# Performance work log

Measured on AMD Instinct MI355X. Metric: run time of the kernel, lower is better.

## Reference

```python
import jax, jax.numpy as jnp
import numpy as np

NUM_GROUPS = 32
EPS = 1e-5


def setup_inputs() -> dict:
    key = jax.random.key(0)
    ks = jax.random.split(key, 11)
    B, C, H, W = 4, 512, 64, 64
    s = 1.0 / np.sqrt(C)
    inp = {
        "x": jax.random.normal(ks[0], (B, C, H, W), dtype=jnp.float32),
        "gn_w": jnp.ones((C,), jnp.float32),
        "gn_b": jnp.zeros((C,), jnp.float32),
        "wq": jax.random.uniform(ks[1], (C, C), jnp.float32, -s, s),
        "bq": jax.random.uniform(ks[2], (C,), jnp.float32, -s, s),
        "wk": jax.random.uniform(ks[3], (C, C), jnp.float32, -s, s),
        "bk": jax.random.uniform(ks[4], (C,), jnp.float32, -s, s),
        "wv": jax.random.uniform(ks[5], (C, C), jnp.float32, -s, s),
        "bv": jax.random.uniform(ks[6], (C,), jnp.float32, -s, s),
        "wo": jax.random.uniform(ks[7], (C, C), jnp.float32, -s, s),
        "bo": jax.random.uniform(ks[8], (C,), jnp.float32, -s, s),
    }
    return inp


def reference(x, gn_w, gn_b, wq, bq, wk, bk, wv, bv, wo, bo):
    B, C, H, W = x.shape
    HW = H * W
    # GroupNorm(32, C)
    g = x.reshape(B, NUM_GROUPS, C // NUM_GROUPS, H, W)
    mu = jnp.mean(g, axis=(2, 3, 4), keepdims=True)
    var = jnp.var(g, axis=(2, 3, 4), keepdims=True)
    h = ((g - mu) * jax.lax.rsqrt(var + EPS)).reshape(B, C, H, W)
    h = h * gn_w[None, :, None, None] + gn_b[None, :, None, None]
    # Faithful to original: .view (reshape), NOT permute -> (B, HW, C)
    h = h.reshape(B, HW, C)
    q = h @ wq.T + bq  # (B, HW, C)
    k = h @ wk.T + bk
    v = h @ wv.T + bv
    # Faithful: reshape (not transpose) to (B, C, HW)
    q = q.reshape(B, C, HW)
    k = k.reshape(B, C, HW)
    v = v.reshape(B, C, HW)
    # attn: (B, HW, HW)
    attn = jnp.einsum('bcn,bcm->bnm', q, k)
    attn = jax.nn.softmax(attn, axis=-1)
    # out: (B, C, HW) = v @ attn^T
    out = jnp.einsum('bcm,bnm->bcn', v, attn)
    # transpose to (B, HW, C), out-proj, then reshape back
    out = jnp.swapaxes(out, 1, 2) @ wo.T + bo
    out = out.reshape(B, C, H, W)
    return out + x
```

## Files before the change

### kernel.cpp

```cpp
#include <hip/hip_runtime.h>
#include <hip/hip_fp16.h>
#include <math.h>

constexpr int BATCH = 4;
constexpr int HWDIM = 4096;
constexpr long CNT   = 2097152;
constexpr long ACNT  = 16777216;
constexpr int GSIZE = 65536;
constexpr float GN_EPS = 1e-5f;

typedef __attribute__((ext_vector_type(8))) _Float16 f16x8;
typedef __attribute__((ext_vector_type(4))) float f32x4;

__device__ __forceinline__ unsigned pkf16(float a, float b) {
  __half ha = __float2half(a), hb = __float2half(b);
  return (unsigned)__half_as_ushort(ha) | ((unsigned)__half_as_ushort(hb) << 16);
}
__device__ __forceinline__ float2 up2(unsigned u) {
  __half2 h = *(__half2*)&u;
  return __half22float2(h);
}
__device__ __forceinline__ void gl_lds16(const void* g, void* l) {
  __builtin_amdgcn_global_load_lds((const __attribute__((address_space(1))) unsigned*)g,
                                   (__attribute__((address_space(3))) unsigned*)l, 16, 0, 0);
}

__global__ void gn_stats_kernel(const float* __restrict__ x,
                                float* __restrict__ mu, float* __restrict__ rs) {
  const int grp = blockIdx.x;
  const float4* p = (const float4*)(x + (long)grp * GSIZE);
  float s = 0.f, q = 0.f;
  for (int i = threadIdx.x; i < GSIZE / 4; i += 256) {
    float4 v = p[i];
    s += (v.x + v.y) + (v.z + v.w);
    q += (v.x * v.x + v.y * v.y) + (v.z * v.z + v.w * v.w);
  }
  #pragma unroll
  for (int o = 32; o > 0; o >>= 1) { s += __shfl_xor(s, o, 64); q += __shfl_xor(q, o, 64); }
  __shared__ float ls[4], lq[4];
  if ((threadIdx.x & 63) == 0) { ls[threadIdx.x >> 6] = s; lq[threadIdx.x >> 6] = q; }
  __syncthreads();
  if (threadIdx.x == 0) {
    float S = (ls[0] + ls[1]) + (ls[2] + ls[3]);
    float Q = (lq[0] + lq[1]) + (lq[2] + lq[3]);
    float m = S * (1.f / GSIZE);
    float var = Q * (1.f / GSIZE) - m * m;
    mu[grp] = m; rs[grp] = rsqrtf(var + GN_EPS);
  }
}

__global__ void gn_norm_f16(const float* __restrict__ x,
                            const float* __restrict__ mu, const float* __restrict__ rs,
                            const float* __restrict__ gw, const float* __restrict__ gb,
                            unsigned short* __restrict__ h) {
  long i = ((long)blockIdx.x * 256 + threadIdx.x) * 4;
  int c   = (int)((i >> 12) & 511);
  int grp = (int)(i >> 16);
  float m = mu[grp], r = rs[grp];
  float w = gw[c] * r;
  float bia = gb[c] - m * w;
  float4 v = *(const float4*)(x + i);
  *(uint2*)(h + i) = (uint2){ pkf16(v.x * w + bia, v.y * w + bia),
                              pkf16(v.z * w + bia, v.w * w + bia) };
}

__global__ void wcvt(const float* __restrict__ w0, const float* __restrict__ w1,
                     const float* __restrict__ w2, const float* __restrict__ w3,
                     unsigned short* __restrict__ o) {
  const float* src = blockIdx.y == 0 ? w0 : blockIdx.y == 1 ? w1 : blockIdx.y == 2 ? w2 : w3;
  long e = ((long)blockIdx.x * 256 + threadIdx.x) * 4;
  float4 v = *(const float4*)(src + e);
  *(uint2*)(o + (long)blockIdx.y * 262144 + e) = (uint2){ pkf16(v.x, v.y), pkf16(v.z, v.w) };
}

__launch_bounds__(256)
__global__ void proj_qkv(const unsigned short* __restrict__ A, const unsigned short* __restrict__ WF,
                         const float* __restrict__ bq, const float* __restrict__ bk,
                         const float* __restrict__ bv, unsigned short* __restrict__ outq) {
  __shared__ __align__(16) unsigned short LB[32768];
  const int z = blockIdx.z;
  const unsigned short* W = WF + (long)z * 262144;
  const float* bias = z == 0 ? bq : z == 1 ? bk : bv;
  unsigned short* outp = outq + (long)z * 8388608;
  const int m0 = blockIdx.x * 128, n0 = blockIdx.y * 128;
  const int t = threadIdx.x, lane = t & 63, w = t >> 6, wm = w & 1, wn = w >> 1;

  f32x4 acc[4][4];
  #pragma unroll
  for (int i = 0; i < 4; i++)
    #pragma unroll
    for (int j = 0; j < 4; j++) acc[i][j] = (f32x4){0.f, 0.f, 0.f, 0.f};

  auto stage = [&](int buf, int k0) {
    unsigned short* As = LB + buf * 16384;
    unsigned short* Bs = As + 8192;
    #pragma unroll
    for (int fbi = 0; fbi < 4; fbi++) {
      int fb = w * 4 + fbi;
      int row = (fb >> 1) * 16 + (lane & 15);
      int g   = (fb & 1) * 4 + (lane >> 4);
      gl_lds16(A + (long)(m0 + row) * 512 + k0 + g * 8, &As[(fb * 64) << 3]);
      gl_lds16(W + (long)(n0 + row) * 512 + k0 + g * 8, &Bs[(fb * 64) << 3]);
    }
  };

  stage(0, 0);
  __syncthreads();
  for (int k0 = 0; k0 < 512; k0 += 64) {
    const int cur = (k0 >> 6) & 1;
    if (k0 + 64 < 512) stage(cur ^ 1, k0 + 64);
    const unsigned short* As = LB + cur * 16384;
    const unsigned short* Bs = As + 8192;
    #pragma unroll
    for (int kk = 0; kk < 2; kk++) {
      f16x8 a[4], b[4];
      #pragma unroll
      for (int i = 0; i < 4; i++)
        a[i] = *(const f16x8*)&As[(((wm * 4 + i) * 2 + kk) * 64 + lane) << 3];
      #pragma unroll
      for (int j = 0; j < 4; j++)
        b[j] = *(const f16x8*)&Bs[(((wn * 4 + j) * 2 + kk) * 64 + lane) << 3];
      #pragma unroll
      for (int i = 0; i < 4; i++)
        #pragma unroll
        for (int j = 0; j < 4; j++)
          acc[i][j] = __builtin_amdgcn_mfma_f32_16x16x32_f16(a[i], b[j], acc[i][j], 0, 0, 0);
    }
    __syncthreads();
  }

  const int lm = lane & 15, quad = lane >> 4;
  #pragma unroll
  for (int i = 0; i < 4; i++)
    #pragma unroll
    for (int j = 0; j < 4; j++) {
      int rr = wm * 64 + i * 16 + quad * 4;
      int cc = wn * 64 + j * 16 + lm;
      float bb = bias[n0 + cc];
      #pragma unroll
      for (int r = 0; r < 4; r++)
        LB[(rr + r) * 136 + cc] = __half_as_ushort(__float2half(acc[i][j][r] + bb));
    }
  __syncthreads();
  #pragma unroll
  for (int k = 0; k < 8; k++) {
    int ro = k * 16 + (t >> 4), col = (t & 15) * 8;
    uint4 vv = *(const uint4*)&LB[ro * 136 + col];
    *(uint4*)(outp + (long)(m0 + ro) * 512 + n0 + col) = vv;
  }
}

__launch_bounds__(256)
__global__ void proj_out(const unsigned short* __restrict__ A, const unsigned short* __restrict__ W,
                         const float* __restrict__ bias, const float* __restrict__ res,
                         float* __restrict__ outv) {
  __shared__ __align__(16) unsigned short LB[32768];
  const int m0 = blockIdx.x * 128, n0 = blockIdx.y * 128;
  const int t = threadIdx.x, lane = t & 63, w = t >> 6, wm = w & 1, wn = w >> 1;

  f32x4 acc[4][4];
  #pragma unroll
  for (int i = 0; i < 4; i++)
    #pragma unroll
    for (int j = 0; j < 4; j++) acc[i][j] = (f32x4){0.f, 0.f, 0.f, 0.f};

  auto stage = [&](int buf, int k0) {
    unsigned short* As = LB + buf * 16384;
    unsigned short* Bs = As + 8192;
    #pragma unroll
    for (int fbi = 0; fbi < 4; fbi++) {
      int fb = w * 4 + fbi;
      int row = (fb >> 1) * 16 + (lane & 15);
      int g   = (fb & 1) * 4 + (lane >> 4);
      gl_lds16(A + (long)(m0 + row) * 512 + k0 + g * 8, &As[(fb * 64) << 3]);
      gl_lds16(W + (long)(n0 + row) * 512 + k0 + g * 8, &Bs[(fb * 64) << 3]);
    }
  };

  stage(0, 0);
  __syncthreads();
  for (int k0 = 0; k0 < 512; k0 += 64) {
    const int cur = (k0 >> 6) & 1;
    if (k0 + 64 < 512) stage(cur ^ 1, k0 + 64);
    const unsigned short* As = LB + cur * 16384;
    const unsigned short* Bs = As + 8192;
    #pragma unroll
    for (int kk = 0; kk < 2; kk++) {
      f16x8 a[4], b[4];
      #pragma unroll
      for (int i = 0; i < 4; i++)
        a[i] = *(const f16x8*)&As[(((wm * 4 + i) * 2 + kk) * 64 + lane) << 3];
      #pragma unroll
      for (int j = 0; j < 4; j++)
        b[j] = *(const f16x8*)&Bs[(((wn * 4 + j) * 2 + kk) * 64 + lane) << 3];
      #pragma unroll
      for (int i = 0; i < 4; i++)
        #pragma unroll
        for (int j = 0; j < 4; j++)
          acc[i][j] = __builtin_amdgcn_mfma_f32_16x16x32_f16(a[i], b[j], acc[i][j], 0, 0, 0);
    }
    __syncthreads();
  }

  const int lm = lane & 15, quad = lane >> 4;
  #pragma unroll
  for (int i = 0; i < 4; i++)
    #pragma unroll
    for (int j = 0; j < 4; j++) {
      int nn = m0 + wm * 64 + i * 16 + quad * 4;
      int cc = n0 + wn * 64 + j * 16 + lm;
      float bb = bias[cc];
      #pragma unroll
      for (int r = 0; r < 4; r++) {
        long idx = (long)(nn + r) * 512 + cc;
        outv[idx] = acc[i][j][r] + bb + res[idx];
      }
    }
}

__global__ void transpose_f16(const unsigned short* __restrict__ qb,
                              const unsigned short* __restrict__ kb,
                              unsigned short* __restrict__ tr) {
  __shared__ __align__(16) unsigned short ld[64 * 72];
  const int zb = blockIdx.z;
  const int b = zb >> 1;
  const unsigned short* in = (zb & 1 ? kb : qb) + (long)b * CNT;
  unsigned short* o = tr + (long)b * 2 * CNT + (zb & 1 ? CNT : 0);
  const int n0 = blockIdx.x * 64, c0 = blockIdx.y * 64;
  const int t = threadIdx.x;
  unsigned* ld32 = (unsigned*)ld;
  {
    const int p = t >> 3, cg = t & 7;
    uint4 r0 = *(const uint4*)(in + (long)(c0 + 2 * p) * 4096 + n0 + 8 * cg);
    uint4 r1 = *(const uint4*)(in + (long)(c0 + 2 * p + 1) * 4096 + n0 + 8 * cg);
    unsigned aw[4] = { r0.x, r0.y, r0.z, r0.w };
    unsigned bw[4] = { r1.x, r1.y, r1.z, r1.w };
    #pragma unroll
    for (int i = 0; i < 4; i++) {
      ld32[(8 * cg + 2 * i) * 36 + p]     = (aw[i] & 0xFFFFu) | (bw[i] << 16);
      ld32[(8 * cg + 2 * i + 1) * 36 + p] = (aw[i] >> 16) | (bw[i] & 0xFFFF0000u);
    }
  }
  __syncthreads();
  {
    const int n = t >> 2, cg2 = t & 3;
    uint4 o0 = *(const uint4*)(ld + n * 72 + 16 * cg2);
    uint4 o1 = *(const uint4*)(ld + n * 72 + 16 * cg2 + 8);
    *(uint4*)(o + (long)(n0 + n) * 512 + c0 + 16 * cg2)     = o0;
    *(uint4*)(o + (long)(n0 + n) * 512 + c0 + 16 * cg2 + 8) = o1;
  }
}

__launch_bounds__(256)
__global__ void qk_f16(const unsigned short* __restrict__ tr, unsigned short* __restrict__ attn) {
  __shared__ __align__(16) unsigned short LB[32768];
  const int b = blockIdx.z;
  const unsigned short* qT = tr + (long)b * 2 * CNT;
  const unsigned short* kT = qT + CNT;
  unsigned short* attnb = attn + (long)b * ACNT;
  const int n0 = blockIdx.x * 128, m0 = blockIdx.y * 128;
  const int t = threadIdx.x, lane = t & 63, w = t >> 6, wm = w & 1, wn = w >> 1;

  f32x4 acc[4][4];
  #pragma unroll
  for (int i = 0; i < 4; i++)
    #pragma unroll
    for (int j = 0; j < 4; j++) acc[i][j] = (f32x4){0.f, 0.f, 0.f, 0.f};

  auto stage = [&](int buf, int k0) {
    unsigned short* As = LB + buf * 16384;
    unsigned short* Bs = As + 8192;
    #pragma unroll
    for (int fbi = 0; fbi < 4; fbi++) {
      int fb = w * 4 + fbi;
      int row = (fb >> 1) * 16 + (lane & 15);
      int g   = (fb & 1) * 4 + (lane >> 4);
      gl_lds16(qT + (long)(n0 + row) * 512 + k0 + g * 8, &As[(fb * 64) << 3]);
      gl_lds16(kT + (long)(m0 + row) * 512 + k0 + g * 8, &Bs[(fb * 64) << 3]);
    }
  };

  stage(0, 0);
  __syncthreads();
  for (int k0 = 0; k0 < 512; k0 += 64) {
    const int cur = (k0 >> 6) & 1;
    if (k0 + 64 < 512) stage(cur ^ 1, k0 + 64);
    const unsigned short* As = LB + cur * 16384;
    const unsigned short* Bs = As + 8192;
    #pragma unroll
    for (int kk = 0; kk < 2; kk++) {
      f16x8 a[4], b[4];
      #pragma unroll
      for (int i = 0; i < 4; i++)
        a[i] = *(const f16x8*)&As[(((wm * 4 + i) * 2 + kk) * 64 + lane) << 3];
      #pragma unroll
      for (int j = 0; j < 4; j++)
        b[j] = *(const f16x8*)&Bs[(((wn * 4 + j) * 2 + kk) * 64 + lane) << 3];
      #pragma unroll
      for (int i = 0; i < 4; i++)
        #pragma unroll
        for (int j = 0; j < 4; j++)
          acc[i][j] = __builtin_amdgcn_mfma_f32_16x16x32_f16(a[i], b[j], acc[i][j], 0, 0, 0);
    }
    __syncthreads();
  }

  const int lm = lane & 15, quad = lane >> 4;
  #pragma unroll
  for (int i = 0; i < 4; i++)
    #pragma unroll
    for (int j = 0; j < 4; j++) {
      int rr = wm * 64 + i * 16 + quad * 4;
      int cc = wn * 64 + j * 16 + lm;
      #pragma unroll
      for (int r = 0; r < 4; r++)
        LB[(rr + r) * 136 + cc] = __half_as_ushort(__float2half(acc[i][j][r]));
    }
  __syncthreads();
  #pragma unroll
  for (int k = 0; k < 8; k++) {
    int ro = k * 16 + (t >> 4), col = (t & 15) * 8;
    uint4 vv = *(const uint4*)&LB[ro * 136 + col];
    *(uint4*)(attnb + (long)(n0 + ro) * 4096 + m0 + col) = vv;
  }
}

__global__ void softmax_f16ip(unsigned short* __restrict__ attn) {
  unsigned short* p = attn + (long)blockIdx.x * HWDIM;
  const int t = threadIdx.x;
  uint4 u0 = *(const uint4*)(p + t * 16);
  uint4 u1 = *(const uint4*)(p + t * 16 + 8);
  float v[16];
  {
    unsigned uu[8] = { u0.x, u0.y, u0.z, u0.w, u1.x, u1.y, u1.z, u1.w };
    #pragma unroll
    for (int i = 0; i < 8; i++) { float2 f = up2(uu[i]); v[2*i] = f.x; v[2*i+1] = f.y; }
  }
  float mx = -1e30f;
  #pragma unroll
  for (int i = 0; i < 16; i++) mx = fmaxf(mx, v[i]);
  #pragma unroll
  for (int o = 32; o > 0; o >>= 1) mx = fmaxf(mx, __shfl_xor(mx, o, 64));
  __shared__ float rmax[4], rsum[4];
  if ((t & 63) == 0) rmax[t >> 6] = mx;
  __syncthreads();
  mx = fmaxf(fmaxf(rmax[0], rmax[1]), fmaxf(rmax[2], rmax[3]));
  float s = 0.f;
  #pragma unroll
  for (int i = 0; i < 16; i++) { v[i] = __expf(v[i] - mx); s += v[i]; }
  #pragma unroll
  for (int o = 32; o > 0; o >>= 1) s += __shfl_xor(s, o, 64);
  if ((t & 63) == 0) rsum[t >> 6] = s;
  __syncthreads();
  s = (rsum[0] + rsum[1]) + (rsum[2] + rsum[3]);
  float inv = 1.f / s;
  uint4 w0, w1;
  w0.x = pkf16(v[0]*inv,  v[1]*inv);  w0.y = pkf16(v[2]*inv,  v[3]*inv);
  w0.z = pkf16(v[4]*inv,  v[5]*inv);  w0.w = pkf16(v[6]*inv,  v[7]*inv);
  w1.x = pkf16(v[8]*inv,  v[9]*inv);  w1.y = pkf16(v[10]*inv, v[11]*inv);
  w1.z = pkf16(v[12]*inv, v[13]*inv); w1.w = pkf16(v[14]*inv, v[15]*inv);
  *(uint4*)(p + t * 16)     = w0;
  *(uint4*)(p + t * 16 + 8) = w1;
}

__launch_bounds__(256)
__global__ void pv_f16(const unsigned short* __restrict__ P, const unsigned short* __restrict__ V,
                       unsigned short* __restrict__ ot) {
  __shared__ __align__(16) unsigned short LB[32768];
  const int b = blockIdx.z;
  const unsigned short* Pb = P + (long)b * ACNT;
  const unsigned short* Vb = V + (long)b * CNT;
  unsigned short* Ob = ot + (long)b * CNT;
  const int n0 = blockIdx.x * 128, c0 = blockIdx.y * 128;
  const int t = threadIdx.x, lane = t & 63, w = t >> 6, wm = w & 1, wn = w >> 1;

  f32x4 acc[4][4];
  #pragma unroll
  for (int i = 0; i < 4; i++)
    #pragma unroll
    for (int j = 0; j < 4; j++) acc[i][j] = (f32x4){0.f, 0.f, 0.f, 0.f};

  auto stage = [&](int buf, int k0) {
    unsigned short* As = LB + buf * 16384;
    unsigned short* Bs = As + 8192;
    #pragma unroll
    for (int fbi = 0; fbi < 4; fbi++) {
      int fb = w * 4 + fbi;
      int row = (fb >> 1) * 16 + (lane & 15);
      int g   = (fb & 1) * 4 + (lane >> 4);
      gl_lds16(Pb + (long)(n0 + row) * 4096 + k0 + g * 8, &As[(fb * 64) << 3]);
      gl_lds16(Vb + (long)(c0 + row) * 4096 + k0 + g * 8, &Bs[(fb * 64) << 3]);
    }
  };

  stage(0, 0);
  __syncthreads();
  for (int k0 = 0; k0 < 4096; k0 += 64) {
    const int cur = (k0 >> 6) & 1;
    if (k0 + 64 < 4096) stage(cur ^ 1, k0 + 64);
    const unsigned short* As = LB + cur * 16384;
    const unsigned short* Bs = As + 8192;
    #pragma unroll
    for (int kk = 0; kk < 2; kk++) {
      f16x8 a[4], b[4];
      #pragma unroll
      for (int i = 0; i < 4; i++)
        a[i] = *(const f16x8*)&As[(((wm * 4 + i) * 2 + kk) * 64 + lane) << 3];
      #pragma unroll
      for (int j = 0; j < 4; j++)
        b[j] = *(const f16x8*)&Bs[(((wn * 4 + j) * 2 + kk) * 64 + lane) << 3];
      #pragma unroll
      for (int i = 0; i < 4; i++)
        #pragma unroll
        for (int j = 0; j < 4; j++)
          acc[i][j] = __builtin_amdgcn_mfma_f32_16x16x32_f16(a[i], b[j], acc[i][j], 0, 0, 0);
    }
    __syncthreads();
  }

  const int lm = lane & 15, quad = lane >> 4;
  #pragma unroll
  for (int i = 0; i < 4; i++)
    #pragma unroll
    for (int j = 0; j < 4; j++) {
      int rr = wm * 64 + i * 16 + quad * 4;
      int cc = wn * 64 + j * 16 + lm;
      #pragma unroll
      for (int r = 0; r < 4; r++)
        LB[(rr + r) * 136 + cc] = __half_as_ushort(__float2half(acc[i][j][r]));
    }
  __syncthreads();
  #pragma unroll
  for (int k = 0; k < 8; k++) {
    int ro = k * 16 + (t >> 4), col = (t & 15) * 8;
    uint4 vv = *(const uint4*)&LB[ro * 136 + col];
    *(uint4*)(Ob + (long)(n0 + ro) * 512 + c0 + col) = vv;
  }
}

extern "C" void kernel_launch(void* const* d_in, const int* in_sizes, int n_in,
                              void* d_out, int out_size, void* d_ws, size_t ws_size,
                              hipStream_t stream) {
  (void)in_sizes; (void)n_in; (void)out_size; (void)ws_size;
  const float* x  = (const float*)d_in[0];
  const float* gw = (const float*)d_in[1];
  const float* gb = (const float*)d_in[2];
  const float* wq = (const float*)d_in[3];
  const float* bq = (const float*)d_in[4];
  const float* wk = (const float*)d_in[5];
  const float* bk = (const float*)d_in[6];
  const float* wv = (const float*)d_in[7];
  const float* bv = (const float*)d_in[8];
  const float* wo = (const float*)d_in[9];
  const float* bo = (const float*)d_in[10];
  float* out = (float*)d_out;

  unsigned short* attn = (unsigned short*)d_ws;
  unsigned short* h    = attn;
  unsigned short* qf   = attn + 4 * ACNT;
  unsigned short* kf   = qf + 8388608;
  unsigned short* vf   = kf + 8388608;
  unsigned short* tr   = vf + 8388608;
  unsigned short* ot   = tr + 16777216;
  unsigned short* wf   = ot + 8388608;
  float* mu = (float*)(wf + 1048576);
  float* rs = mu + 128;

  gn_stats_kernel<<<dim3(128), dim3(256), 0, stream>>>(x, mu, rs);
  gn_norm_f16<<<dim3(8192), dim3(256), 0, stream>>>(x, mu, rs, gw, gb, h);
  wcvt<<<dim3(256, 4), dim3(256), 0, stream>>>(wq, wk, wv, wo, wf);

  proj_qkv<<<dim3(128, 4, 3), 256, 0, stream>>>(h, wf, bq, bk, bv, qf);

  transpose_f16<<<dim3(64, 8, 8), 256, 0, stream>>>(qf, kf, tr);
  qk_f16<<<dim3(32, 32, 4), 256, 0, stream>>>(tr, attn);
  softmax_f16ip<<<dim3(16384), 256, 0, stream>>>(attn);
  pv_f16<<<dim3(32, 4, 4), 256, 0, stream>>>(attn, vf, ot);

  proj_out<<<dim3(128, 4), 256, 0, stream>>>(ot, wf + 786432, bo, x, out);
}
```

Before: 539.8 us.

## Share a prefetch-two-ahead GEMM core and swizzle block order for L2 reuse

Moves the four MFMA GEMM kernels onto a shared templated core. The core keeps two stages of global-to-LDS loads in flight, uses explicit vmcnt waits and raw barriers, and has a peeled tail. This is meant to hide global load latency behind MFMA work that the old loop exposed on every iteration. qk_f16 and pv_f16 also remap block indices so that consecutively scheduled blocks share input tiles, which should improve L2 hit rates. The hand-written waitcnt counts and barrier placement are fragile and could cause LDS races if the in-flight load count assumption is wrong.

```diff
diff --git a/kernel.cpp b/kernel.cpp
--- a/kernel.cpp
+++ b/kernel.cpp
@@ -73,6 +73,68 @@
   *(uint2*)(o + (long)blockIdx.y * 262144 + e) = (uint2){ pkf16(v.x, v.y), pkf16(v.z, v.w) };
 }
 
+template<int K>
+__device__ __forceinline__ void gemm_core(const unsigned short* __restrict__ Ab, long sA,
+                                          const unsigned short* __restrict__ Bb, long sB,
+                                          unsigned short* LB, const int t, f32x4 (&acc)[4][4]) {
+  const int lane = t & 63, w = t >> 6, wm = w & 1, wn = w >> 1;
+
+  auto stage = [&](int buf, int k0) {
+    unsigned short* S = LB + buf * 16384;
+    #pragma unroll
+    for (int fbi = 0; fbi < 4; fbi++) {
+      int fb = w * 4 + fbi;
+      int row = (fb >> 1) * 16 + (lane & 15);
+      int g   = (fb & 1) * 4 + (lane >> 4);
+      gl_lds16(Ab + (long)row * sA + k0 + g * 8, &S[(fb * 64) << 3]);
+      gl_lds16(Bb + (long)row * sB + k0 + g * 8, &S[8192 + ((fb * 64) << 3)]);
+    }
+  };
+  auto compute = [&](int buf) {
+    const unsigned short* As = LB + buf * 16384;
+    const unsigned short* Bs = As + 8192;
+    #pragma unroll
+    for (int kk = 0; kk < 2; kk++) {
+      f16x8 a[4], b[4];
+      #pragma unroll
+      for (int i = 0; i < 4; i++)
+        a[i] = *(const f16x8*)&As[(((wm * 4 + i) * 2 + kk) * 64 + lane) << 3];
+      #pragma unroll
+      for (int j = 0; j < 4; j++)
+        b[j] = *(const f16x8*)&Bs[(((wn * 4 + j) * 2 + kk) * 64 + lane) << 3];
+      #pragma unroll
+      for (int i = 0; i < 4; i++)
+        #pragma unroll
+        for (int j = 0; j < 4; j++)
+          acc[i][j] = __builtin_amdgcn_mfma_f32_16x16x32_f16(a[i], b[j], acc[i][j], 0, 0, 0);
+    }
+  };
+
+  stage(0, 0);
+  stage(1, 64);
+  asm volatile("s_waitcnt vmcnt(8)" ::: "memory");
+  __builtin_amdgcn_s_barrier();
+  __builtin_amdgcn_sched_barrier(0);
+
+  #pragma unroll 1
+  for (int k0 = 0; k0 + 192 <= K; k0 += 64) {
+    const int cur = (k0 >> 6) & 1;
+    compute(cur);
+    __builtin_amdgcn_sched_barrier(0);
+    __builtin_amdgcn_s_barrier();
+    stage(cur, k0 + 128);
+    asm volatile("s_waitcnt vmcnt(8)" ::: "memory");
+    __builtin_amdgcn_s_barrier();
+    __builtin_amdgcn_sched_barrier(0);
+  }
+  compute(((K - 128) >> 6) & 1);
+  asm volatile("s_waitcnt vmcnt(0)" ::: "memory");
+  __builtin_amdgcn_s_barrier();
+  __builtin_amdgcn_sched_barrier(0);
+  compute(((K - 64) >> 6) & 1);
+  __syncthreads();
+}
+
 __launch_bounds__(256)
 __global__ void proj_qkv(const unsigned short* __restrict__ A, const unsigned short* __restrict__ WF,
                          const float* __restrict__ bq, const float* __restrict__ bk,
@@ -83,7 +145,7 @@
   const float* bias = z == 0 ? bq : z == 1 ? bk : bv;
   unsigned short* outp = outq + (long)z * 8388608;
   const int m0 = blockIdx.x * 128, n0 = blockIdx.y * 128;
-  const int t = threadIdx.x, lane = t & 63, w = t >> 6, wm = w & 1, wn = w >> 1;
+  const int t = threadIdx.x;
 
   f32x4 acc[4][4];
   #pragma unroll
@@ -91,44 +153,9 @@
     #pragma unroll
     for (int j = 0; j < 4; j++) acc[i][j] = (f32x4){0.f, 0.f, 0.f, 0.f};
 
-  auto stage = [&](int buf, int k0) {
-    unsigned short* As = LB + buf * 16384;
-    unsigned short* Bs = As + 8192;
-    #pragma unroll
-    for (int fbi = 0; fbi < 4; fbi++) {
-      int fb = w * 4 + fbi;
-      int row = (fb >> 1) * 16 + (lane & 15);
-      int g   = (fb & 1) * 4 + (lane >> 4);
-      gl_lds16(A + (long)(m0 + row) * 512 + k0 + g * 8, &As[(fb * 64) << 3]);
-      gl_lds16(W + (long)(n0 + row) * 512 + k0 + g * 8, &Bs[(fb * 64) << 3]);
-    }
-  };
-
-  stage(0, 0);
-  __syncthreads();
-  for (int k0 = 0; k0 < 512; k0 += 64) {
-    const int cur = (k0 >> 6) & 1;
-    if (k0 + 64 < 512) stage(cur ^ 1, k0 + 64);
-    const unsigned short* As = LB + cur * 16384;
-    const unsigned short* Bs = As + 8192;
-    #pragma unroll
-    for (int kk = 0; kk < 2; kk++) {
-      f16x8 a[4], b[4];
-      #pragma unroll
-      for (int i = 0; i < 4; i++)
-        a[i] = *(const f16x8*)&As[(((wm * 4 + i) * 2 + kk) * 64 + lane) << 3];
-      #pragma unroll
-      for (int j = 0; j < 4; j++)
-        b[j] = *(const f16x8*)&Bs[(((wn * 4 + j) * 2 + kk) * 64 + lane) << 3];
-      #pragma unroll
-      for (int i = 0; i < 4; i++)
-        #pragma unroll
-        for (int j = 0; j < 4; j++)
-          acc[i][j] = __builtin_amdgcn_mfma_f32_16x16x32_f16(a[i], b[j], acc[i][j], 0, 0, 0);
-    }
-    __syncthreads();
-  }
-
+  gemm_core<512>(A + (long)m0 * 512, 512, W + (long)n0 * 512, 512, LB, t, acc);
+
+  const int lane = t & 63, w = t >> 6, wm = w & 1, wn = w >> 1;
   const int lm = lane & 15, quad = lane >> 4;
   #pragma unroll
   for (int i = 0; i < 4; i++)
@@ -156,7 +183,7 @@
                          float* __restrict__ outv) {
   __shared__ __align__(16) unsigned short LB[32768];
   const int m0 = blockIdx.x * 128, n0 = blockIdx.y * 128;
-  const int t = threadIdx.x, lane = t & 63, w = t >> 6, wm = w & 1, wn = w >> 1;
+  const int t = threadIdx.x;
 
   f32x4 acc[4][4];
   #pragma unroll
@@ -164,44 +191,9 @@
     #pragma unroll
     for (int j = 0; j < 4; j++) acc[i][j] = (f32x4){0.f, 0.f, 0.f, 0.f};
 
-  auto stage = [&](int buf, int k0) {
-    unsigned short* As = LB + buf * 16384;
-    unsigned short* Bs = As + 8192;
-    #pragma unroll
-    for (int fbi = 0; fbi < 4; fbi++) {
-      int fb = w * 4 + fbi;
-      int row = (fb >> 1) * 16 + (lane & 15);
-      int g   = (fb & 1) * 4 + (lane >> 4);
-      gl_lds16(A + (long)(m0 + row) * 512 + k0 + g * 8, &As[(fb * 64) << 3]);
-      gl_lds16(W + (long)(n0 + row) * 512 + k0 + g * 8, &Bs[(fb * 64) << 3]);
-    }
-  };
-
-  stage(0, 0);
-  __syncthreads();
-  for (int k0 = 0; k0 < 512; k0 += 64) {
-    const int cur = (k0 >> 6) & 1;
-    if (k0 + 64 < 512) stage(cur ^ 1, k0 + 64);
-    const unsigned short* As = LB + cur * 16384;
-    const unsigned short* Bs = As + 8192;
-    #pragma unroll
-    for (int kk = 0; kk < 2; kk++) {
-      f16x8 a[4], b[4];
-      #pragma unroll
-      for (int i = 0; i < 4; i++)
-        a[i] = *(const f16x8*)&As[(((wm * 4 + i) * 2 + kk) * 64 + lane) << 3];
-      #pragma unroll
-      for (int j = 0; j < 4; j++)
-        b[j] = *(const f16x8*)&Bs[(((wn * 4 + j) * 2 + kk) * 64 + lane) << 3];
-      #pragma unroll
-      for (int i = 0; i < 4; i++)
-        #pragma unroll
-        for (int j = 0; j < 4; j++)
-          acc[i][j] = __builtin_amdgcn_mfma_f32_16x16x32_f16(a[i], b[j], acc[i][j], 0, 0, 0);
-    }
-    __syncthreads();
-  }
-
+  gemm_core<512>(A + (long)m0 * 512, 512, W + (long)n0 * 512, 512, LB, t, acc);
+
+  const int lane = t & 63, w = t >> 6, wm = w & 1, wn = w >> 1;
   const int lm = lane & 15, quad = lane >> 4;
   #pragma unroll
   for (int i = 0; i < 4; i++)
@@ -254,12 +246,14 @@
 __launch_bounds__(256)
 __global__ void qk_f16(const unsigned short* __restrict__ tr, unsigned short* __restrict__ attn) {
   __shared__ __align__(16) unsigned short LB[32768];
-  const int b = blockIdx.z;
+  const int lin = blockIdx.x + 32 * blockIdx.y + 1024 * blockIdx.z;
+  const int nl = (lin & 7) * 512 + (lin >> 3);
+  const int b = nl >> 10, by = (nl >> 5) & 31, bx = nl & 31;
   const unsigned short* qT = tr + (long)b * 2 * CNT;
   const unsigned short* kT = qT + CNT;
   unsigned short* attnb = attn + (long)b * ACNT;
-  const int n0 = blockIdx.x * 128, m0 = blockIdx.y * 128;
-  const int t = threadIdx.x, lane = t & 63, w = t >> 6, wm = w & 1, wn = w >> 1;
+  const int n0 = bx * 128, m0 = by * 128;
+  const int t = threadIdx.x;
 
   f32x4 acc[4][4];
   #pragma unroll
@@ -267,44 +261,9 @@
     #pragma unroll
     for (int j = 0; j < 4; j++) acc[i][j] = (f32x4){0.f, 0.f, 0.f, 0.f};
 
-  auto stage = [&](int buf, int k0) {
-    unsigned short* As = LB + buf * 16384;
-    unsigned short* Bs = As + 8192;
-    #pragma unroll
-    for (int fbi = 0; fbi < 4; fbi++) {
-      int fb = w * 4 + fbi;
-      int row = (fb >> 1) * 16 + (lane & 15);
-      int g   = (fb & 1) * 4 + (lane >> 4);
-      gl_lds16(qT + (long)(n0 + row) * 512 + k0 + g * 8, &As[(fb * 64) << 3]);
-      gl_lds16(kT + (long)(m0 + row) * 512 + k0 + g * 8, &Bs[(fb * 64) << 3]);
-    }
-  };
-
-  stage(0, 0);
-  __syncthreads();
-  for (int k0 = 0; k0 < 512; k0 += 64) {
-    const int cur = (k0 >> 6) & 1;
-    if (k0 + 64 < 512) stage(cur ^ 1, k0 + 64);
-    const unsigned short* As = LB + cur * 16384;
-    const unsigned short* Bs = As + 8192;
-    #pragma unroll
-    for (int kk = 0; kk < 2; kk++) {
-      f16x8 a[4], b[4];
-      #pragma unroll
-      for (int i = 0; i < 4; i++)
-        a[i] = *(const f16x8*)&As[(((wm * 4 + i) * 2 + kk) * 64 + lane) << 3];
-      #pragma unroll
-      for (int j = 0; j < 4; j++)
-        b[j] = *(const f16x8*)&Bs[(((wn * 4 + j) * 2 + kk) * 64 + lane) << 3];
-      #pragma unroll
-      for (int i = 0; i < 4; i++)
-        #pragma unroll
-        for (int j = 0; j < 4; j++)
-          acc[i][j] = __builtin_amdgcn_mfma_f32_16x16x32_f16(a[i], b[j], acc[i][j], 0, 0, 0);
-    }
-    __syncthreads();
-  }
-
+  gemm_core<512>(qT + (long)n0 * 512, 512, kT + (long)m0 * 512, 512, LB, t, acc);
+
+  const int lane = t & 63, w = t >> 6, wm = w & 1, wn = w >> 1;
   const int lm = lane & 15, quad = lane >> 4;
   #pragma unroll
   for (int i = 0; i < 4; i++)
@@ -367,12 +326,14 @@
 __global__ void pv_f16(const unsigned short* __restrict__ P, const unsigned short* __restrict__ V,
                        unsigned short* __restrict__ ot) {
   __shared__ __align__(16) unsigned short LB[32768];
-  const int b = blockIdx.z;
+  const int lin = blockIdx.x + 32 * blockIdx.y + 128 * blockIdx.z;
+  const int nl = (lin & 7) * 64 + (lin >> 3);
+  const int bx = nl & 31, by = (nl >> 5) & 3, b = nl >> 7;
   const unsigned short* Pb = P + (long)b * ACNT;
   const unsigned short* Vb = V + (long)b * CNT;
   unsigned short* Ob = ot + (long)b * CNT;
-  const int n0 = blockIdx.x * 128, c0 = blockIdx.y * 128;
-  const int t = threadIdx.x, lane = t & 63, w = t >> 6, wm = w & 1, wn = w >> 1;
+  const int n0 = bx * 128, c0 = by * 128;
+  const int t = threadIdx.x;
 
   f32x4 acc[4][4];
   #pragma unroll
@@ -380,44 +341,9 @@
     #pragma unroll
     for (int j = 0; j < 4; j++) acc[i][j] = (f32x4){0.f, 0.f, 0.f, 0.f};
 
-  auto stage = [&](int buf, int k0) {
-    unsigned short* As = LB + buf * 16384;
-    unsigned short* Bs = As + 8192;
-    #pragma unroll
-    for (int fbi = 0; fbi < 4; fbi++) {
-      int fb = w * 4 + fbi;
-      int row = (fb >> 1) * 16 + (lane & 15);
-      int g   = (fb & 1) * 4 + (lane >> 4);
-      gl_lds16(Pb + (long)(n0 + row) * 4096 + k0 + g * 8, &As[(fb * 64) << 3]);
-      gl_lds16(Vb + (long)(c0 + row) * 4096 + k0 + g * 8, &Bs[(fb * 64) << 3]);
-    }
-  };
-
-  stage(0, 0);
-  __syncthreads();
-  for (int k0 = 0; k0 < 4096; k0 += 64) {
-    const int cur = (k0 >> 6) & 1;
-    if (k0 + 64 < 4096) stage(cur ^ 1, k0 + 64);
-    const unsigned short* As = LB + cur * 16384;
-    const unsigned short* Bs = As + 8192;
-    #pragma unroll
-    for (int kk = 0; kk < 2; kk++) {
-      f16x8 a[4], b[4];
-      #pragma unroll
-      for (int i = 0; i < 4; i++)
-        a[i] = *(const f16x8*)&As[(((wm * 4 + i) * 2 + kk) * 64 + lane) << 3];
-      #pragma unroll
-      for (int j = 0; j < 4; j++)
-        b[j] = *(const f16x8*)&Bs[(((wn * 4 + j) * 2 + kk) * 64 + lane) << 3];
-      #pragma unroll
-      for (int i = 0; i < 4; i++)
-        #pragma unroll
-        for (int j = 0; j < 4; j++)
-          acc[i][j] = __builtin_amdgcn_mfma_f32_16x16x32_f16(a[i], b[j], acc[i][j], 0, 0, 0);
-    }
-    __syncthreads();
-  }
-
+  gemm_core<4096>(Pb + (long)n0 * 4096, 4096, Vb + (long)c0 * 4096, 4096, LB, t, acc);
+
+  const int lane = t & 63, w = t >> 6, wm = w & 1, wn = w >> 1;
   const int lm = lane & 15, quad = lane >> 4;
   #pragma unroll
   for (int i = 0; i < 4; i++)
```

New measurement: 512.2 us. -5.1%, faster.
